# Kernel optimization log

Measured on AMD Instinct MI355X. Metric: run time of the kernel, lower is better.

## Reference

```python
import jax, jax.numpy as jnp
import numpy as np

WORD_THRES = 0.2
COS_EPS = 1e-8
NEG_INF = -1e9


def setup_inputs() -> dict:
    key = jax.random.key(0)
    k1, k2, k3, k4 = jax.random.split(key, 4)
    B, L, V, E, A = 1024, 256, 50000, 300, 30
    inputs = jax.random.randint(k1, (B, L), 0, V)            # token ids, 0 == pad
    w_emb = jax.random.normal(k2, (V, E), dtype=jnp.float32) * 0.1
    a_emb = jax.random.normal(k3, (A, E), dtype=jnp.float32)
    a_weight = jax.random.uniform(k4, (A,), dtype=jnp.float32)
    return {"inputs": inputs, "w_emb": w_emb, "a_emb": a_emb, "a_weight": a_weight}


def reference(inputs, w_emb, a_emb, a_weight):
    # inputs: [B, L] int ids; w_emb: [V, E]; a_emb: [A, E]; a_weight: [A]
    inputs_len = (inputs != 0).sum(axis=1).astype(jnp.float32)      # [B]
    x_wrd = w_emb[inputs]                                            # [B, L, E]

    # cosine similarity between each aspect and each word (torch semantics:
    # dot / (max(||a||, eps) * max(||x||, eps)))
    a_norm = jnp.maximum(jnp.linalg.norm(a_emb, axis=-1), COS_EPS)   # [A]
    x_norm = jnp.maximum(jnp.linalg.norm(x_wrd, axis=-1), COS_EPS)   # [B, L]
    dot = jnp.einsum("ae,ble->abl", a_emb, x_wrd)                    # [A, B, L]
    sim = dot / (a_norm[:, None, None] * x_norm[None, :, :])

    # Threshold(word_thres, 0): x if x > thres else 0, then scale by aspect weight
    sim = jnp.where(sim > WORD_THRES, sim, 0.0) * a_weight[:, None, None]

    # centroid score: relu(sim).max over aspects, summed over seq, length-normalized
    centroid = jnp.maximum(sim, 0.0).max(axis=0)                     # [B, L]
    centroid_score = centroid.sum(axis=1) / (inputs_len + 1e-5)      # [B]

    # attention: mask exact zeros to -1e9, max over aspects, softmax over seq
    sim_m = jnp.where(sim == 0.0, NEG_INF, sim)
    scores = sim_m.max(axis=0)                                       # [B, L]
    a = jax.nn.softmax(scores, axis=1)                               # [B, L]

    z = jnp.einsum("bl,ble->be", a, x_wrd)                           # [B, E]
    enc_out = z * (centroid_score > 1e-4).astype(z.dtype)[:, None]
    return enc_out, a, centroid_score
```

## Files before the change

### kernel.cpp

```cpp
#include <hip/hip_runtime.h>
#include <math.h>

#define BB 1024
#define LL 256
#define VV 50000
#define EE 300
#define AA 30
#define WORD_THRES 0.2f
#define COS_EPS_F 1e-8f
#define NEG_INF_F -1e9f

__global__ void __launch_bounds__(256) cent_kernel(
    const float* __restrict__ w_emb,
    const float* __restrict__ a_emb,
    const float* __restrict__ a_weight,
    float* __restrict__ cent)
{
    __shared__ float4 s_a[AA * 75];
    __shared__ float s_scale[AA];
    __shared__ float s_aw[AA];

    const int t = threadIdx.x;
    const float4* __restrict__ a4 = (const float4*)a_emb;

    for (int s = t; s < AA * 75; s += 256) s_a[s] = a4[s];

    {
        const int a = t >> 3, j = t & 7;
        if (a < AA) {
            float n2a = 0.f;
            for (int c = j; c < 75; c += 8) {
                const float4 x = a4[a * 75 + c];
                n2a += x.x * x.x + x.y * x.y + x.z * x.z + x.w * x.w;
            }
            n2a += __shfl_xor(n2a, 1);
            n2a += __shfl_xor(n2a, 2);
            n2a += __shfl_xor(n2a, 4);
            if (j == 0) {
                s_scale[a] = 1.f / fmaxf(sqrtf(n2a), COS_EPS_F);
                s_aw[a] = a_weight[a];
            }
        }
    }
    __syncthreads();

    const int p = t & 3;
    const int slot = t >> 2;
    const int v0 = blockIdx.x * 128 + slot;
    const int v1 = v0 + 64;
    const bool ok1 = v1 < VV;
    const float* __restrict__ r0 = w_emb + (size_t)v0 * EE;
    const float* __restrict__ r1 = w_emb + (size_t)(ok1 ? v1 : 0) * EE;

    float acc0[AA], acc1[AA];
#pragma unroll
    for (int a = 0; a < AA; ++a) { acc0[a] = 0.f; acc1[a] = 0.f; }
    float n20 = 0.f, n21 = 0.f;

    for (int k = 0; k < 18; ++k) {
        const int j = 4 * k + p;
        const float4 w0 = *(const float4*)(r0 + 4 * j);
        const float4 w1 = *(const float4*)(r1 + 4 * j);
        n20 += w0.x * w0.x + w0.y * w0.y + w0.z * w0.z + w0.w * w0.w;
        n21 += w1.x * w1.x + w1.y * w1.y + w1.z * w1.z + w1.w * w1.w;
        const float4* __restrict__ ap = s_a + j;
#pragma unroll
        for (int a = 0; a < AA; ++a) {
            const float4 av = ap[a * 75];
            acc0[a] = fmaf(av.x, w0.x, fmaf(av.y, w0.y,
                      fmaf(av.z, w0.z, fmaf(av.w, w0.w, acc0[a]))));
            acc1[a] = fmaf(av.x, w1.x, fmaf(av.y, w1.y,
                      fmaf(av.z, w1.z, fmaf(av.w, w1.w, acc1[a]))));
        }
    }
    if (p < 3) {
        const int j = 72 + p;
        const float4 w0 = *(const float4*)(r0 + 4 * j);
        const float4 w1 = *(const float4*)(r1 + 4 * j);
        n20 += w0.x * w0.x + w0.y * w0.y + w0.z * w0.z + w0.w * w0.w;
        n21 += w1.x * w1.x + w1.y * w1.y + w1.z * w1.z + w1.w * w1.w;
        const float4* __restrict__ ap = s_a + j;
#pragma unroll
        for (int a = 0; a < AA; ++a) {
            const float4 av = ap[a * 75];
            acc0[a] = fmaf(av.x, w0.x, fmaf(av.y, w0.y,
                      fmaf(av.z, w0.z, fmaf(av.w, w0.w, acc0[a]))));
            acc1[a] = fmaf(av.x, w1.x, fmaf(av.y, w1.y,
                      fmaf(av.z, w1.z, fmaf(av.w, w1.w, acc1[a]))));
        }
    }

#pragma unroll
    for (int a = 0; a < AA; ++a) {
        acc0[a] += __shfl_xor(acc0[a], 1); acc0[a] += __shfl_xor(acc0[a], 2);
        acc1[a] += __shfl_xor(acc1[a], 1); acc1[a] += __shfl_xor(acc1[a], 2);
    }
    n20 += __shfl_xor(n20, 1); n20 += __shfl_xor(n20, 2);
    n21 += __shfl_xor(n21, 1); n21 += __shfl_xor(n21, 2);

    if (p == 0) {
        const float inv_x0 = 1.f / fmaxf(sqrtf(n20), COS_EPS_F);
        const float inv_x1 = 1.f / fmaxf(sqrtf(n21), COS_EPS_F);
        float m0 = 0.f, m1 = 0.f;
#pragma unroll
        for (int a = 0; a < AA; ++a) {
            const float c0 = acc0[a] * s_scale[a] * inv_x0;
            const float c1 = acc1[a] * s_scale[a] * inv_x1;
            m0 = fmaxf(m0, (c0 > WORD_THRES) ? c0 * s_aw[a] : 0.f);
            m1 = fmaxf(m1, (c1 > WORD_THRES) ? c1 * s_aw[a] : 0.f);
        }
        cent[v0] = m0;
        if (ok1) cent[v1] = m1;
    }
}

__global__ void __launch_bounds__(256) row_kernel(
    const int* __restrict__ inputs,
    const float* __restrict__ w_emb,
    const float* __restrict__ cent,
    float* __restrict__ out)
{
    const int b = blockIdx.x;
    const int t = threadIdx.x;
    const int wid = t >> 6, lane = t & 63;

    __shared__ float pA[4], pB[4], pC[4], pD[4];
    __shared__ int s_nact;
    __shared__ int s_act_id[LL];
    __shared__ float s_act_w[LL];

    const int id = inputs[b * LL + t];
    const float c = cent[id];
    const float score = (c > 0.f) ? c : NEG_INF_F;
    const float cnt = (id != 0) ? 1.f : 0.f;
    if (t == 0) s_nact = 0;

    float s1 = c, s2 = cnt, s3 = score;
#pragma unroll
    for (int o = 32; o > 0; o >>= 1) {
        s1 += __shfl_down(s1, o);
        s2 += __shfl_down(s2, o);
        s3 = fmaxf(s3, __shfl_down(s3, o));
    }
    if (lane == 0) { pA[wid] = s1; pB[wid] = s2; pC[wid] = s3; }
    __syncthreads();

    const float sum_c = pA[0] + pA[1] + pA[2] + pA[3];
    const float len   = pB[0] + pB[1] + pB[2] + pB[3];
    const float mx    = fmaxf(fmaxf(pC[0], pC[1]), fmaxf(pC[2], pC[3]));

    const float p = expf(score - mx);
    float s4 = p;
#pragma unroll
    for (int o = 32; o > 0; o >>= 1) s4 += __shfl_down(s4, o);
    if (lane == 0) pD[wid] = s4;
    __syncthreads();
    const float sum_p = pD[0] + pD[1] + pD[2] + pD[3];

    const float a_l = p / sum_p;
    const float cs = sum_c / (len + 1e-5f);
    const float gate = (cs > 1e-4f) ? 1.f : 0.f;

    out[BB * EE + b * LL + t] = a_l;
    if (t == 0) out[BB * EE + BB * LL + b] = cs;

    if (score > -1e8f) {
        const int i = atomicAdd(&s_nact, 1);
        s_act_id[i] = id;
        s_act_w[i] = a_l;
    }
    __syncthreads();
    const int n = s_nact;

    if (t < EE / 4) {
        float4 acc = {0.f, 0.f, 0.f, 0.f};
        for (int i = 0; i < n; ++i) {
            const float wgt = s_act_w[i];
            const float4 r = *(const float4*)(w_emb + (size_t)s_act_id[i] * EE + 4 * t);
            acc.x += wgt * r.x; acc.y += wgt * r.y;
            acc.z += wgt * r.z; acc.w += wgt * r.w;
        }
        acc.x *= gate; acc.y *= gate; acc.z *= gate; acc.w *= gate;
        *(float4*)(out + b * EE + 4 * t) = acc;
    }
}

extern "C" void kernel_launch(void* const* d_in, const int* in_sizes, int n_in,
                              void* d_out, int out_size, void* d_ws, size_t ws_size,
                              hipStream_t stream) {
    const int* inputs = (const int*)d_in[0];
    const float* w_emb = (const float*)d_in[1];
    const float* a_emb = (const float*)d_in[2];
    const float* a_weight = (const float*)d_in[3];
    float* out = (float*)d_out;
    float* cent = (float*)d_ws;

    cent_kernel<<<(VV + 127) / 128, 256, 0, stream>>>(w_emb, a_emb, a_weight, cent);
    row_kernel<<<BB, 256, 0, stream>>>(inputs, w_emb, cent, out);
}
```

Baseline: 126.6 us.

## Fuse vocab scoring and row pass into cooperative MFMA kernel with split-bf16

Result: slower. 183.8 us (+45.2%).

```diff
diff --git a/kernel.cpp b/kernel.cpp
--- a/kernel.cpp
+++ b/kernel.cpp
@@ -1,5 +1,8 @@
 #include <hip/hip_runtime.h>
+#include <hip/hip_cooperative_groups.h>
 #include <math.h>
+
+namespace cg = cooperative_groups;
 
 #define BB 1024
 #define LL 256
@@ -9,109 +12,302 @@
 #define WORD_THRES 0.2f
 #define COS_EPS_F 1e-8f
 #define NEG_INF_F -1e9f
-
-__global__ void __launch_bounds__(256) cent_kernel(
+#define RECHECK_DELTA 2e-4f
+#define CGRID 256
+#define NTILES 782
+
+typedef __attribute__((ext_vector_type(8))) short bf16x8;
+typedef __attribute__((ext_vector_type(4))) float f32x4;
+
+#define MFMA16(a, b, c) __builtin_amdgcn_mfma_f32_16x16x32_bf16((a), (b), (c), 0, 0, 0)
+
+__device__ __forceinline__ void gld_lds16(const float* g, float* l) {
+    typedef const __attribute__((address_space(1))) void* gas_p;
+    typedef __attribute__((address_space(3))) void* las_p;
+    __builtin_amdgcn_global_load_lds((gas_p)g, (las_p)l, 16, 0, 0);
+}
+
+__device__ __forceinline__ unsigned pack_hi(float a, float b) {
+    return (__float_as_uint(a) >> 16) | (__float_as_uint(b) & 0xFFFF0000u);
+}
+__device__ __forceinline__ float hi_part(float a) {
+    return __uint_as_float(__float_as_uint(a) & 0xFFFF0000u);
+}
+__device__ __forceinline__ void cvt_hilo(const float4 f0, const float4 f1,
+                                         uint4& uh, uint4& ul) {
+    uh.x = pack_hi(f0.x, f0.y);
+    uh.y = pack_hi(f0.z, f0.w);
+    uh.z = pack_hi(f1.x, f1.y);
+    uh.w = pack_hi(f1.z, f1.w);
+    const float l0 = f0.x - hi_part(f0.x), l1 = f0.y - hi_part(f0.y);
+    const float l2 = f0.z - hi_part(f0.z), l3 = f0.w - hi_part(f0.w);
+    const float l4 = f1.x - hi_part(f1.x), l5 = f1.y - hi_part(f1.y);
+    const float l6 = f1.z - hi_part(f1.z), l7 = f1.w - hi_part(f1.w);
+    ul.x = pack_hi(l0, l1);
+    ul.y = pack_hi(l2, l3);
+    ul.z = pack_hi(l4, l5);
+    ul.w = pack_hi(l6, l7);
+}
+
+__device__ __forceinline__ void stage16(const float* __restrict__ w_emb,
+                                        int tile, int w, int lane, float* dst) {
+    const float* gend = w_emb + (size_t)VV * EE - 4;
+    const float* g = w_emb + ((size_t)tile * 64 + w * 16) * EE;
+    float* d = dst + w * 4800;
+#pragma unroll
+    for (int i = 0; i < 19; ++i) {
+        if (i < 18 || lane < 48) {
+            const int off = i * 256 + lane * 4;
+            const float* src = g + off;
+            if (src > gend) src = gend;
+            gld_lds16(src, d + off);
+        }
+    }
+}
+
+#define CENT_BODY(w_emb, a_emb, a_weight, cent)                                \
+    const int t = threadIdx.x;                                                 \
+    const int l = t & 63;                                                      \
+    const int w = t >> 6;                                                      \
+    const int m = l & 15;                                                      \
+    const int kg = l >> 4;                                                     \
+    {         \
+        const int a = t >> 3, j = t & 7;                                       \
+        if (a < AA) {                                                          \
+            const float4* a4 = (const float4*)a_emb + a * 75;                  \
+            float n2a = 0.f;                                                   \
+            for (int c = j; c < 75; c += 8) {                                  \
+                const float4 x = a4[c];                                        \
+                n2a += x.x * x.x + x.y * x.y + x.z * x.z + x.w * x.w;          \
+            }                                                                  \
+            n2a += __shfl_xor(n2a, 1);                                         \
+            n2a += __shfl_xor(n2a, 2);                                         \
+            n2a += __shfl_xor(n2a, 4);                                         \
+            if (j == 0) {                                                      \
+                s_scale[a] = 1.f / fmaxf(sqrtf(n2a), COS_EPS_F);               \
+                s_aw[a] = a_weight[a];                                         \
+            }                                                                  \
+        }                                                                      \
+        if (t == 30 || t == 31) { s_scale[t] = 0.f; s_aw[t] = 0.f; }           \
+    }                                                                          \
+    {                        \
+        uint4* s_bfrag = s_pool;                                               \
+        for (int ks = w; ks < 10; ks += 4) {                                   \
+            const int kb = kg * 8 + 32 * ks;                                   \
+            _Pragma("unroll")                                                  \
+            for (int tt = 0; tt < 2; ++tt) {                                   \
+                const int col = tt * 16 + m;                                   \
+                float4 f0 = {0.f,0.f,0.f,0.f}, f1 = {0.f,0.f,0.f,0.f};         \
+                if (col < AA) {                                                \
+                    const float* ap = a_emb + col * EE;                        \
+                    if (kb <= 296) f0 = *(const float4*)(ap + kb);             \
+                    if (kb <= 292) f1 = *(const float4*)(ap + kb + 4);         \
+                }                                                              \
+                uint4 uh, ul;                                                  \
+                cvt_hilo(f0, f1, uh, ul);                                      \
+                s_bfrag[(ks * 4 + tt * 2 + 0) * 64 + l] = uh;                  \
+                s_bfrag[(ks * 4 + tt * 2 + 1) * 64 + l] = ul;                  \
+            }                                                                  \
+        }                                                                      \
+    }                                                                          \
+    __syncthreads();                                                           \
+    bf16x8 bfr[40];                                                            \
+    _Pragma("unroll")                                                          \
+    for (int q = 0; q < 40; ++q)                                               \
+        bfr[q] = __builtin_bit_cast(bf16x8, s_pool[q * 64 + l]);               \
+    __syncthreads();                                                           \
+    float* buf0 = (float*)s_pool;                                              \
+    float* buf1 = buf0 + 19200;                                                \
+    const float sc0 = s_scale[m], aw0 = s_aw[m];                               \
+    const float sc1 = s_scale[16 + m], aw1 = s_aw[16 + m];                     \
+    const bool col1ok = (16 + m) < AA;                                         \
+    int cur = 0;                                                               \
+    int tile = blockIdx.x;                                                     \
+    stage16(w_emb, tile, w, l, buf0);                                          \
+    for (; tile < NTILES; tile += CGRID) {                                     \
+        const int nxt = tile + CGRID;                                          \
+        float* bufc = cur ? buf1 : buf0;                                       \
+        if (nxt < NTILES) {                                                    \
+            stage16(w_emb, nxt, w, l, cur ? buf0 : buf1);                      \
+            asm volatile("s_waitcnt vmcnt(19)" ::: "memory");                  \
+        } else {                                                               \
+            asm volatile("s_waitcnt vmcnt(0)" ::: "memory");                   \
+        }                                                                      \
+        const float* arow = bufc + w * 4800 + m * 300;                         \
+        f32x4 acc0 = {0.f, 0.f, 0.f, 0.f};                                     \
+        f32x4 acc1 = {0.f, 0.f, 0.f, 0.f};                                     \
+        float n2 = 0.f;                                                        \
+        _Pragma("unroll")                                                      \
+        for (int i = 0; i < 10; ++i) {                                         \
+            const int kb = kg * 8 + 32 * i;                                    \
+            float4 f0 = *(const float4*)(arow + kb);                           \
+            float4 f1 = *(const float4*)(arow + kb + 4);                       \
+            if (i == 9) {                                                      \
+                const float4 z = {0.f, 0.f, 0.f, 0.f};                         \
+                if (kg >= 2) f0 = z;                                           \
+                if (kg >= 1) f1 = z;                                           \
+            }                                                                  \
+            n2 = fmaf(f0.x,f0.x, fmaf(f0.y,f0.y, fmaf(f0.z,f0.z,               \
+                 fmaf(f0.w,f0.w, n2))));                                       \
+            n2 = fmaf(f1.x,f1.x, fmaf(f1.y,f1.y, fmaf(f1.z,f1.z,               \
+                 fmaf(f1.w,f1.w, n2))));                                       \
+            uint4 uh, ul;                                                      \
+            cvt_hilo(f0, f1, uh, ul);                                          \
+            const bf16x8 ah = __builtin_bit_cast(bf16x8, uh);                  \
+            const bf16x8 al = __builtin_bit_cast(bf16x8, ul);                  \
+            acc0 = MFMA16(ah, bfr[i * 4 + 0], acc0);                           \
+            acc1 = MFMA16(ah, bfr[i * 4 + 2], acc1);                           \
+            acc0 = MFMA16(ah, bfr[i * 4 + 1], acc0);                           \
+            acc1 = MFMA16(ah, bfr[i * 4 + 3], acc1);                           \
+            acc0 = MFMA16(al, bfr[i * 4 + 0], acc0);                           \
+            acc1 = MFMA16(al, bfr[i * 4 + 2], acc1);                           \
+        }                                                                      \
+        n2 += __shfl_xor(n2, 16);                                              \
+        n2 += __shfl_xor(n2, 32);                                              \
+        const int vtile = tile * 64 + w * 16;                                  \
+        float mx[4];                                                           \
+        _Pragma("unroll")                                                      \
+        for (int j = 0; j < 4; ++j) {                                          \
+            const int r = kg * 4 + j;                                          \
+            const float n2r = __int_as_float(                                  \
+                __builtin_amdgcn_ds_bpermute(r << 2, __float_as_int(n2)));     \
+            const float inv_x = 1.f / fmaxf(sqrtf(n2r), COS_EPS_F);            \
+            float c0 = acc0[j] * sc0 * inv_x;                                  \
+            float c1 = acc1[j] * sc1 * inv_x;                                  \
+            if (fabsf(c0 - WORD_THRES) < RECHECK_DELTA) {                      \
+                const float* wr = bufc + w * 4800 + r * 300;                   \
+                const float* ar = a_emb + m * EE;                              \
+                float d = 0.f;                                                 \
+                for (int k = 0; k < EE; ++k) d = fmaf(wr[k], ar[k], d);        \
+                c0 = d * sc0 * inv_x;                                          \
+            }                                                                  \
+            if (col1ok && fabsf(c1 - WORD_THRES) < RECHECK_DELTA) {            \
+                const float* wr = bufc + w * 4800 + r * 300;                   \
+                const float* ar = a_emb + (16 + m) * EE;                       \
+                float d = 0.f;                                                 \
+                for (int k = 0; k < EE; ++k) d = fmaf(wr[k], ar[k], d);        \
+                c1 = d * sc1 * inv_x;                                          \
+            }                                                                  \
+            float mj = fmaxf((c0 > WORD_THRES) ? c0 * aw0 : 0.f,               \
+                             (c1 > WORD_THRES) ? c1 * aw1 : 0.f);              \
+            mj = fmaxf(mj, __shfl_xor(mj, 1));                                 \
+            mj = fmaxf(mj, __shfl_xor(mj, 2));                                 \
+            mj = fmaxf(mj, __shfl_xor(mj, 4));                                 \
+            mj = fmaxf(mj, __shfl_xor(mj, 8));                                 \
+            mx[j] = mj;                                                        \
+        }                                                                      \
+        if (m == 0 && vtile < VV) {                                            \
+            const float4 o = {mx[0], mx[1], mx[2], mx[3]};                     \
+            *(float4*)(cent + vtile + kg * 4) = o;                             \
+        }                                                                      \
+        cur ^= 1;                                                              \
+    }
+
+#define ROW_BODY(w_emb, cent, out, brow, id4, lane, w, s_id, s_w, s_n)         \
+  {                                                                            \
+    if (lane == 0) s_n[w] = 0;                                                 \
+    const float rc0 = cent[id4.x];                                             \
+    const float rc1 = cent[id4.y];                                             \
+    const float rc2 = cent[id4.z];                                             \
+    const float rc3 = cent[id4.w];                                             \
+    const float rsc0 = (rc0 > 0.f) ? rc0 : NEG_INF_F;                          \
+    const float rsc1 = (rc1 > 0.f) ? rc1 : NEG_INF_F;                          \
+    const float rsc2 = (rc2 > 0.f) ? rc2 : NEG_INF_F;                          \
+    const float rsc3 = (rc3 > 0.f) ? rc3 : NEG_INF_F;                          \
+    float s1 = rc0 + rc1 + rc2 + rc3;                                          \
+    float s2 = (id4.x != 0 ? 1.f : 0.f) + (id4.y != 0 ? 1.f : 0.f) +           \
+               (id4.z != 0 ? 1.f : 0.f) + (id4.w != 0 ? 1.f : 0.f);            \
+    float s3 = fmaxf(fmaxf(rsc0, rsc1), fmaxf(rsc2, rsc3));                    \
+    _Pragma("unroll")                                                          \
+    for (int o = 1; o < 64; o <<= 1) {                                         \
+        s1 += __shfl_xor(s1, o);                                               \
+        s2 += __shfl_xor(s2, o);                                               \
+        s3 = fmaxf(s3, __shfl_xor(s3, o));                                     \
+    }                                                                          \
+    const float mxv = s3;                                                      \
+    const float p0 = expf(rsc0 - mxv);                                         \
+    const float p1 = expf(rsc1 - mxv);                                         \
+    const float p2 = expf(rsc2 - mxv);                                         \
+    const float p3 = expf(rsc3 - mxv);                                         \
+    float s4 = p0 + p1 + p2 + p3;                                              \
+    _Pragma("unroll")                                                          \
+    for (int o = 1; o < 64; o <<= 1) s4 += __shfl_xor(s4, o);                  \
+    const float rinv = 1.f / s4;                                               \
+    const float4 av = {p0 * rinv, p1 * rinv, p2 * rinv, p3 * rinv};            \
+    *(float4*)(out + BB * EE + brow * LL + lane * 4) = av;                     \
+    const float cs = s1 / (s2 + 1e-5f);                                        \
+    const float gate = (cs > 1e-4f) ? 1.f : 0.f;                               \
+    if (lane == 0) out[BB * EE + BB * LL + brow] = cs;                         \
+    if (rsc0 > -1e8f) { const int i = atomicAdd(&s_n[w], 1);                   \
+        s_id[w * LL + i] = id4.x; s_w[w * LL + i] = av.x; }                    \
+    if (rsc1 > -1e8f) { const int i = atomicAdd(&s_n[w], 1);                   \
+        s_id[w * LL + i] = id4.y; s_w[w * LL + i] = av.y; }                    \
+    if (rsc2 > -1e8f) { const int i = atomicAdd(&s_n[w], 1);                   \
+        s_id[w * LL + i] = id4.z; s_w[w * LL + i] = av.z; }                    \
+    if (rsc3 > -1e8f) { const int i = atomicAdd(&s_n[w], 1);                   \
+        s_id[w * LL + i] = id4.w; s_w[w * LL + i] = av.w; }                    \
+    __syncthreads();                                                           \
+    const int n = s_n[w];                                                      \
+    float4 accA = {0.f, 0.f, 0.f, 0.f};                                        \
+    float4 accB = {0.f, 0.f, 0.f, 0.f};                                        \
+    for (int i = 0; i < n; ++i) {                                              \
+        const float wgt = s_w[w * LL + i];                                     \
+        const float4* rp = (const float4*)(w_emb + (size_t)s_id[w*LL+i] * EE); \
+        const float4 ra = rp[lane];                                            \
+        accA.x += wgt * ra.x; accA.y += wgt * ra.y;                            \
+        accA.z += wgt * ra.z; accA.w += wgt * ra.w;                            \
+        if (lane < 11) {                                                       \
+            const float4 rb = rp[64 + lane];                                   \
+            accB.x += wgt * rb.x; accB.y += wgt * rb.y;                        \
+            accB.z += wgt * rb.z; accB.w += wgt * rb.w;                        \
+        }                                                                      \
+    }                                                                          \
+    accA.x *= gate; accA.y *= gate; accA.z *= gate; accA.w *= gate;            \
+    *(float4*)(out + brow * EE + 4 * lane) = accA;                             \
+    if (lane < 11) {                                                           \
+        accB.x *= gate; accB.y *= gate; accB.z *= gate; accB.w *= gate;        \
+        *(float4*)(out + brow * EE + 256 + 4 * lane) = accB;                   \
+    }                                                                          \
+  }
+
+__global__ void __launch_bounds__(256, 1) fused_kernel(
+    const int* __restrict__ inputs,
+    const float* __restrict__ w_emb,
+    const float* __restrict__ a_emb,
+    const float* __restrict__ a_weight,
+    float* __restrict__ cent,
+    float* __restrict__ out)
+{
+    __shared__ uint4 s_pool[9600];
+    __shared__ float s_scale[32];
+    __shared__ float s_aw[32];
+
+    CENT_BODY(w_emb, a_emb, a_weight, cent)
+
+    const int brow = blockIdx.x * 4 + w;
+    const int4 id4 = *(const int4*)(inputs + brow * LL + l * 4);
+
+    __threadfence();
+    cg::this_grid().sync();
+    __syncthreads();
+
+    int* p2_id = (int*)s_pool;
+    float* p2_w = (float*)s_pool + 1024;
+    int* p2_n = (int*)s_pool + 2048;
+
+    ROW_BODY(w_emb, cent, out, brow, id4, l, w, p2_id, p2_w, p2_n)
+}
+
+__global__ void __launch_bounds__(256, 1) cent_kernel(
     const float* __restrict__ w_emb,
     const float* __restrict__ a_emb,
     const float* __restrict__ a_weight,
     float* __restrict__ cent)
 {
-    __shared__ float4 s_a[AA * 75];
-    __shared__ float s_scale[AA];
-    __shared__ float s_aw[AA];
-
-    const int t = threadIdx.x;
-    const float4* __restrict__ a4 = (const float4*)a_emb;
-
-    for (int s = t; s < AA * 75; s += 256) s_a[s] = a4[s];
-
-    {
-        const int a = t >> 3, j = t & 7;
-        if (a < AA) {
-            float n2a = 0.f;
-            for (int c = j; c < 75; c += 8) {
-                const float4 x = a4[a * 75 + c];
-                n2a += x.x * x.x + x.y * x.y + x.z * x.z + x.w * x.w;
-            }
-            n2a += __shfl_xor(n2a, 1);
-            n2a += __shfl_xor(n2a, 2);
-            n2a += __shfl_xor(n2a, 4);
-            if (j == 0) {
-                s_scale[a] = 1.f / fmaxf(sqrtf(n2a), COS_EPS_F);
-                s_aw[a] = a_weight[a];
-            }
-        }
-    }
-    __syncthreads();
-
-    const int p = t & 3;
-    const int slot = t >> 2;
-    const int v0 = blockIdx.x * 128 + slot;
-    const int v1 = v0 + 64;
-    const bool ok1 = v1 < VV;
-    const float* __restrict__ r0 = w_emb + (size_t)v0 * EE;
-    const float* __restrict__ r1 = w_emb + (size_t)(ok1 ? v1 : 0) * EE;
-
-    float acc0[AA], acc1[AA];
-#pragma unroll
-    for (int a = 0; a < AA; ++a) { acc0[a] = 0.f; acc1[a] = 0.f; }
-    float n20 = 0.f, n21 = 0.f;
-
-    for (int k = 0; k < 18; ++k) {
-        const int j = 4 * k + p;
-        const float4 w0 = *(const float4*)(r0 + 4 * j);
-        const float4 w1 = *(const float4*)(r1 + 4 * j);
-        n20 += w0.x * w0.x + w0.y * w0.y + w0.z * w0.z + w0.w * w0.w;
-        n21 += w1.x * w1.x + w1.y * w1.y + w1.z * w1.z + w1.w * w1.w;
-        const float4* __restrict__ ap = s_a + j;
-#pragma unroll
-        for (int a = 0; a < AA; ++a) {
-            const float4 av = ap[a * 75];
-            acc0[a] = fmaf(av.x, w0.x, fmaf(av.y, w0.y,
-                      fmaf(av.z, w0.z, fmaf(av.w, w0.w, acc0[a]))));
-            acc1[a] = fmaf(av.x, w1.x, fmaf(av.y, w1.y,
-                      fmaf(av.z, w1.z, fmaf(av.w, w1.w, acc1[a]))));
-        }
-    }
-    if (p < 3) {
-        const int j = 72 + p;
-        const float4 w0 = *(const float4*)(r0 + 4 * j);
-        const float4 w1 = *(const float4*)(r1 + 4 * j);
-        n20 += w0.x * w0.x + w0.y * w0.y + w0.z * w0.z + w0.w * w0.w;
-        n21 += w1.x * w1.x + w1.y * w1.y + w1.z * w1.z + w1.w * w1.w;
-        const float4* __restrict__ ap = s_a + j;
-#pragma unroll
-        for (int a = 0; a < AA; ++a) {
-            const float4 av = ap[a * 75];
-            acc0[a] = fmaf(av.x, w0.x, fmaf(av.y, w0.y,
-                      fmaf(av.z, w0.z, fmaf(av.w, w0.w, acc0[a]))));
-            acc1[a] = fmaf(av.x, w1.x, fmaf(av.y, w1.y,
-                      fmaf(av.z, w1.z, fmaf(av.w, w1.w, acc1[a]))));
-        }
-    }
-
-#pragma unroll
-    for (int a = 0; a < AA; ++a) {
-        acc0[a] += __shfl_xor(acc0[a], 1); acc0[a] += __shfl_xor(acc0[a], 2);
-        acc1[a] += __shfl_xor(acc1[a], 1); acc1[a] += __shfl_xor(acc1[a], 2);
-    }
-    n20 += __shfl_xor(n20, 1); n20 += __shfl_xor(n20, 2);
-    n21 += __shfl_xor(n21, 1); n21 += __shfl_xor(n21, 2);
-
-    if (p == 0) {
-        const float inv_x0 = 1.f / fmaxf(sqrtf(n20), COS_EPS_F);
-        const float inv_x1 = 1.f / fmaxf(sqrtf(n21), COS_EPS_F);
-        float m0 = 0.f, m1 = 0.f;
-#pragma unroll
-        for (int a = 0; a < AA; ++a) {
-            const float c0 = acc0[a] * s_scale[a] * inv_x0;
-            const float c1 = acc1[a] * s_scale[a] * inv_x1;
-            m0 = fmaxf(m0, (c0 > WORD_THRES) ? c0 * s_aw[a] : 0.f);
-            m1 = fmaxf(m1, (c1 > WORD_THRES) ? c1 * s_aw[a] : 0.f);
-        }
-        cent[v0] = m0;
-        if (ok1) cent[v1] = m1;
-    }
+    __shared__ uint4 s_pool[9600];
+    __shared__ float s_scale[32];
+    __shared__ float s_aw[32];
+    CENT_BODY(w_emb, a_emb, a_weight, cent)
 }
 
 __global__ void __launch_bounds__(256) row_kernel(
@@ -120,69 +316,14 @@
     const float* __restrict__ cent,
     float* __restrict__ out)
 {
-    const int b = blockIdx.x;
-    const int t = threadIdx.x;
-    const int wid = t >> 6, lane = t & 63;
-
-    __shared__ float pA[4], pB[4], pC[4], pD[4];
-    __shared__ int s_nact;
-    __shared__ int s_act_id[LL];
-    __shared__ float s_act_w[LL];
-
-    const int id = inputs[b * LL + t];
-    const float c = cent[id];
-    const float score = (c > 0.f) ? c : NEG_INF_F;
-    const float cnt = (id != 0) ? 1.f : 0.f;
-    if (t == 0) s_nact = 0;
-
-    float s1 = c, s2 = cnt, s3 = score;
-#pragma unroll
-    for (int o = 32; o > 0; o >>= 1) {
-        s1 += __shfl_down(s1, o);
-        s2 += __shfl_down(s2, o);
-        s3 = fmaxf(s3, __shfl_down(s3, o));
-    }
-    if (lane == 0) { pA[wid] = s1; pB[wid] = s2; pC[wid] = s3; }
-    __syncthreads();
-
-    const float sum_c = pA[0] + pA[1] + pA[2] + pA[3];
-    const float len   = pB[0] + pB[1] + pB[2] + pB[3];
-    const float mx    = fmaxf(fmaxf(pC[0], pC[1]), fmaxf(pC[2], pC[3]));
-
-    const float p = expf(score - mx);
-    float s4 = p;
-#pragma unroll
-    for (int o = 32; o > 0; o >>= 1) s4 += __shfl_down(s4, o);
-    if (lane == 0) pD[wid] = s4;
-    __syncthreads();
-    const float sum_p = pD[0] + pD[1] + pD[2] + pD[3];
-
-    const float a_l = p / sum_p;
-    const float cs = sum_c / (len + 1e-5f);
-    const float gate = (cs > 1e-4f) ? 1.f : 0.f;
-
-    out[BB * EE + b * LL + t] = a_l;
-    if (t == 0) out[BB * EE + BB * LL + b] = cs;
-
-    if (score > -1e8f) {
-        const int i = atomicAdd(&s_nact, 1);
-        s_act_id[i] = id;
-        s_act_w[i] = a_l;
-    }
-    __syncthreads();
-    const int n = s_nact;
-
-    if (t < EE / 4) {
-        float4 acc = {0.f, 0.f, 0.f, 0.f};
-        for (int i = 0; i < n; ++i) {
-            const float wgt = s_act_w[i];
-            const float4 r = *(const float4*)(w_emb + (size_t)s_act_id[i] * EE + 4 * t);
-            acc.x += wgt * r.x; acc.y += wgt * r.y;
-            acc.z += wgt * r.z; acc.w += wgt * r.w;
-        }
-        acc.x *= gate; acc.y *= gate; acc.z *= gate; acc.w *= gate;
-        *(float4*)(out + b * EE + 4 * t) = acc;
-    }
+    __shared__ int s_id[4 * LL];
+    __shared__ float s_w[4 * LL];
+    __shared__ int s_n[4];
+    const int w = threadIdx.x >> 6;
+    const int lane = threadIdx.x & 63;
+    const int brow = blockIdx.x * 4 + w;
+    const int4 id4 = *(const int4*)(inputs + brow * LL + lane * 4);
+    ROW_BODY(w_emb, cent, out, brow, id4, lane, w, s_id, s_w, s_n)
 }
 
 extern "C" void kernel_launch(void* const* d_in, const int* in_sizes, int n_in,
@@ -195,6 +336,25 @@
     float* out = (float*)d_out;
     float* cent = (float*)d_ws;
 
-    cent_kernel<<<(VV + 127) / 128, 256, 0, stream>>>(w_emb, a_emb, a_weight, cent);
-    row_kernel<<<BB, 256, 0, stream>>>(inputs, w_emb, cent, out);
-}
+    static int coop = -1;
+    if (coop < 0) {
+        int dev = 0;
+        (void)hipGetDevice(&dev);
+        if (hipDeviceGetAttribute(&coop, hipDeviceAttributeCooperativeLaunch,
+                                  dev) != hipSuccess)
+            coop = 0;
+    }
+
+    bool launched = false;
+    if (coop) {
+        void* args[] = {(void*)&inputs, (void*)&w_emb, (void*)&a_emb,
+                        (void*)&a_weight, (void*)&cent, (void*)&out};
+        if (hipLaunchCooperativeKernel((const void*)fused_kernel, dim3(CGRID),
+                                       dim3(256), args, 0, stream) == hipSuccess)
+            launched = true;
+    }
+    if (!launched) {
+        cent_kernel<<<CGRID, 256, 0, stream>>>(w_emb, a_emb, a_weight, cent);
+        row_kernel<<<BB / 4, 256, 0, stream>>>(inputs, w_emb, cent, out);
+    }
+}
```
